# Kernel tuning notes

Measured on AMD Instinct MI355X. Metric: run time of the kernel, lower is better.

The kernel has to match this reference:

```python
import jax, jax.numpy as jnp
import numpy as np

BS, EMB, RES = 256, 768, 14
N_MASKS, HID, OUT, N_PROJ = 16, 4096, 256, 4
BN_EPS = 1e-5


def setup_inputs() -> dict:
    key = jax.random.key(0)
    ks = jax.random.split(key, 8)
    x = jax.random.normal(ks[0], (BS, EMB, RES, RES), jnp.float32)
    # binary ROI masks over the 14x14 = 196 patch grid
    masks = (jax.random.uniform(ks[1], (BS, N_MASKS, RES * RES)) < 0.3).astype(jnp.float32)
    projection_idx = jax.random.randint(ks[2], (N_MASKS,), 0, N_PROJ, jnp.int32)
    mask_ids = jax.random.randint(ks[3], (BS, N_MASKS), 0, 100, jnp.int32)
    # stacked params for the N_PROJ MLP projectors
    W1 = jax.random.normal(ks[4], (N_PROJ, EMB, HID), jnp.float32) * 0.02
    b1 = jnp.zeros((N_PROJ, HID), jnp.float32)
    gamma = jnp.ones((N_PROJ, HID), jnp.float32)
    beta = jnp.zeros((N_PROJ, HID), jnp.float32)
    W2 = jax.random.normal(ks[5], (N_PROJ, HID, OUT), jnp.float32) * 0.02
    b2 = jnp.zeros((N_PROJ, OUT), jnp.float32)
    return {"x": x, "masks": masks, "projection_idx": projection_idx,
            "mask_ids": mask_ids, "W1": W1, "b1": b1, "gamma": gamma,
            "beta": beta, "W2": W2, "b2": b2}


def reference(x, masks, projection_idx, mask_ids, W1, b1, gamma, beta, W2, b2):
    bs, emb, hx, hy = x.shape
    # [bs, emb, hx, hy] -> [bs, hw, emb]
    emb_local = jnp.transpose(x, (0, 2, 3, 1)).reshape(bs, hx * hy, emb)
    # mask-normalized pooling:  pooled[b,n,:] = mean of embeddings inside mask n
    area = masks.sum(axis=-1, keepdims=True)
    smpl = masks / jnp.maximum(area, 1.0)
    pooled = smpl @ emb_local                       # [bs, n_masks, emb]
    # dense dispatch: run EVERY projector over all pooled tokens (as original)
    h = jnp.einsum('bne,peh->pbnh', pooled, W1) + b1[:, None, None, :]
    # BatchNorm1d in training mode over flattened (bs*n_masks) batch, per projector
    mu = h.mean(axis=(1, 2), keepdims=True)
    var = jnp.mean(jnp.square(h - mu), axis=(1, 2), keepdims=True)  # biased var
    h = (h - mu) * jax.lax.rsqrt(var + BN_EPS) * gamma[:, None, None, :] + beta[:, None, None, :]
    h = jax.nn.relu(h)
    o = jnp.einsum('pbnh,pho->pbno', h, W2) + b2[:, None, None, :]   # [P, bs, n, out]
    # keep only projector projection_idx[n] for mask-slot n (disjoint selection)
    n_proj = W1.shape[0]
    sel = (projection_idx[None, :] == jnp.arange(n_proj)[:, None]).astype(o.dtype)  # [P, n]
    xs = (o * sel[:, None, :, None]).sum(axis=0)     # [bs, n_masks, out]
    return (xs, mask_ids)
```

## Files before the change

### kernel.cpp

```cpp
#include <hip/hip_runtime.h>
#include <hip/hip_bf16.h>

#define BS 256
#define EMB 768
#define HW 196
#define NMASK 16
#define HID 4096
#define OUT 256
#define NPROJ 4
#define MROWS 4096

typedef __attribute__((ext_vector_type(8))) short bf16x8;
typedef __attribute__((ext_vector_type(4))) float f32x4;
typedef __attribute__((ext_vector_type(8))) unsigned short u16x8;

__device__ inline float bf2f(unsigned short u) {
    unsigned int x = ((unsigned int)u) << 16;
    return __builtin_bit_cast(float, x);
}
__device__ inline short f2bfs(float f) {
    return __builtin_bit_cast(short, __float2bfloat16(f));
}

#define GL16(gptr, lptr)                                                     \
    __builtin_amdgcn_global_load_lds(                                        \
        (const __attribute__((address_space(1))) void*)(gptr),               \
        (__attribute__((address_space(3))) void*)(lptr), 16, 0, 0)

__global__ __launch_bounds__(256) void pool_mfma(
    const float* __restrict__ x, const float* __restrict__ masks,
    __hip_bfloat16* __restrict__ pooledG)
{
    __shared__ __align__(16) short afr[7 * 64 * 8];
    __shared__ float inv[NMASK];
    const int ec = blockIdx.x, b = blockIdx.y, tid = threadIdx.x;
    const float* mb = masks + (size_t)b * NMASK * HW;

    for (int s = tid; s < 7 * 64; s += 256) {
        int m = s & 15, kb = ((s >> 4) & 3) * 8 + (s >> 6) * 32;
        short v[8];
        #pragma unroll
        for (int j = 0; j < 8; ++j) {
            int kk = kb + j;
            v[j] = (kk < HW) ? f2bfs(mb[m * HW + kk]) : (short)0;
        }
        #pragma unroll
        for (int j = 0; j < 8; ++j) afr[s * 8 + j] = v[j];
    }
    if (tid >= 192) {
        int l = tid - 192, m = l >> 2, q = l & 3;
        float a = 0.f;
        for (int hw = q; hw < HW; hw += 4) a += mb[m * HW + hw];
        a += __shfl_xor(a, 1);
        a += __shfl_xor(a, 2);
        if (q == 0) inv[m] = 1.0f / fmaxf(a, 1.0f);
    }
    __syncthreads();

    const int lane = tid & 63, w = tid >> 6;
    const int lc = lane & 15, l4 = lane >> 4;
    const int ebase = ec * 192 + w * 48;
    const bf16x8* afv = (const bf16x8*)afr;
    f32x4 acc[3] = {};

    const float* xb0 = x + ((size_t)b * EMB + ebase + lc) * HW;

    for (int kc = 0; kc < 6; ++kc) {
        bf16x8 af = afv[kc * 64 + lane];
        float4 u[3][2];
        #pragma unroll
        for (int t = 0; t < 3; ++t) {
            const float* xr = xb0 + (size_t)(t * 16) * HW + kc * 32 + l4 * 8;
            u[t][0] = *(const float4*)(xr);
            u[t][1] = *(const float4*)(xr + 4);
        }
        #pragma unroll
        for (int t = 0; t < 3; ++t) {
            bf16x8 bf;
            bf[0] = f2bfs(u[t][0].x); bf[1] = f2bfs(u[t][0].y);
            bf[2] = f2bfs(u[t][0].z); bf[3] = f2bfs(u[t][0].w);
            bf[4] = f2bfs(u[t][1].x); bf[5] = f2bfs(u[t][1].y);
            bf[6] = f2bfs(u[t][1].z); bf[7] = f2bfs(u[t][1].w);
            acc[t] = __builtin_amdgcn_mfma_f32_16x16x32_bf16(af, bf, acc[t], 0, 0, 0);
        }
    }
    {
        bf16x8 af = afv[6 * 64 + lane];
        #pragma unroll
        for (int t = 0; t < 3; ++t) {
            bf16x8 bf = {};
            if (l4 == 0) {
                float4 u0 = *(const float4*)(xb0 + (size_t)(t * 16) * HW + 192);
                bf[0] = f2bfs(u0.x); bf[1] = f2bfs(u0.y);
                bf[2] = f2bfs(u0.z); bf[3] = f2bfs(u0.w);
            }
            acc[t] = __builtin_amdgcn_mfma_f32_16x16x32_bf16(af, bf, acc[t], 0, 0, 0);
        }
    }

    #pragma unroll
    for (int t = 0; t < 3; ++t) {
        int e = ebase + t * 16 + lc;
        #pragma unroll
        for (int j = 0; j < 4; ++j) {
            int m = l4 * 4 + j;
            pooledG[((size_t)m * 256 + b) * EMB + e] =
                __float2bfloat16(acc[t][j] * inv[m]);
        }
    }
}

__global__ __launch_bounds__(256) void transpose_cvt(
    const float* __restrict__ src, __hip_bfloat16* __restrict__ dst, int R, int C)
{
    __shared__ float tile[64][65];
    const float* s = src + (size_t)blockIdx.z * R * C;
    __hip_bfloat16* d = dst + (size_t)blockIdx.z * R * C;
    const int c0 = blockIdx.x * 64, r0 = blockIdx.y * 64, tid = threadIdx.x;
    for (int i = tid; i < 4096; i += 256) {
        int r = i >> 6, c = i & 63;
        tile[r][c] = s[(size_t)(r0 + r) * C + c0 + c];
    }
    __syncthreads();
    for (int i = tid; i < 4096; i += 256) {
        int c = i >> 6, r = i & 63;
        d[(size_t)(c0 + c) * R + r0 + r] = __float2bfloat16(tile[r][c]);
    }
}

__global__ __launch_bounds__(256) void transpose_pg(
    const __hip_bfloat16* __restrict__ src, __hip_bfloat16* __restrict__ dst)
{
    __shared__ __hip_bfloat16 tile[64][65];
    const int c0 = blockIdx.x * 64, r0 = blockIdx.y * 64, tid = threadIdx.x;
    for (int i = tid; i < 4096; i += 256) {
        int r = i >> 6, c = i & 63;
        tile[r][c] = src[(size_t)(r0 + r) * EMB + c0 + c];
    }
    __syncthreads();
    for (int i = tid; i < 4096; i += 256) {
        int c = i >> 6, r = i & 63;
        dst[(size_t)(c0 + c) * MROWS + r0 + r] = tile[r][c];
    }
}

__global__ __launch_bounds__(256) void meanpool(
    const __hip_bfloat16* __restrict__ PT, float* __restrict__ mp)
{
    const int e = blockIdx.x, tid = threadIdx.x;
    const u16x8* p = (const u16x8*)(PT + (size_t)e * MROWS);
    u16x8 v1 = p[tid], v2 = p[tid + 256];
    float s = 0.f;
    #pragma unroll
    for (int j = 0; j < 8; ++j) s += bf2f((unsigned short)v1[j]) + bf2f((unsigned short)v2[j]);
    #pragma unroll
    for (int o = 1; o < 64; o <<= 1) s += __shfl_xor(s, o);
    __shared__ float wsum[4];
    if ((tid & 63) == 0) wsum[tid >> 6] = s;
    __syncthreads();
    if (tid == 0) mp[e] = (wsum[0] + wsum[1] + wsum[2] + wsum[3]) * (1.0f / 4096.0f);
}

__global__ __launch_bounds__(256) void cgemm(
    const __hip_bfloat16* __restrict__ PT, float* __restrict__ Cf)
{
    __shared__ __align__(16) __hip_bfloat16 As[128 * 32];
    __shared__ __align__(16) __hip_bfloat16 Bs[128 * 32];
    const int tid = threadIdx.x, lane = tid & 63, wid = tid >> 6;
    const int n0 = blockIdx.x * 128, m0 = blockIdx.y * 128, kbase = blockIdx.z * 512;
    const int wr = wid >> 1, wc = wid & 1;
    const int l4 = lane >> 4, lc = lane & 15;

    f32x4 acc[4][4] = {};
    for (int k0 = kbase; k0 < kbase + 512; k0 += 32) {
        __syncthreads();
        #pragma unroll
        for (int r = 0; r < 2; ++r) {
            int t = r * 256 + tid;
            int row = t >> 2, ko = (t & 3) * 8;
            GL16(PT + (size_t)(m0 + row) * MROWS + k0 + ko, &As[(r * 256 + wid * 64) * 8]);
        }
        #pragma unroll
        for (int r = 0; r < 2; ++r) {
            int t = r * 256 + tid;
            int row = t >> 2, ko = (t & 3) * 8;
            GL16(PT + (size_t)(n0 + row) * MROWS + k0 + ko, &Bs[(r * 256 + wid * 64) * 8]);
        }
        __syncthreads();
        const bf16x8* Av = (const bf16x8*)As;
        const bf16x8* Bv = (const bf16x8*)Bs;
        bf16x8 a[4], b[4];
        #pragma unroll
        for (int m = 0; m < 4; ++m) a[m] = Av[(wr * 64 + m * 16 + lc) * 4 + l4];
        #pragma unroll
        for (int n = 0; n < 4; ++n) b[n] = Bv[(wc * 64 + n * 16 + lc) * 4 + l4];
        #pragma unroll
        for (int m = 0; m < 4; ++m)
            #pragma unroll
            for (int n = 0; n < 4; ++n)
                acc[m][n] = __builtin_amdgcn_mfma_f32_16x16x32_bf16(a[m], b[n], acc[m][n], 0, 0, 0);
    }
    #pragma unroll
    for (int m = 0; m < 4; ++m)
        #pragma unroll
        for (int n = 0; n < 4; ++n)
            #pragma unroll
            for (int j = 0; j < 4; ++j) {
                int row = m0 + wr * 64 + m * 16 + l4 * 4 + j;
                int col = n0 + wc * 64 + n * 16 + lc;
                atomicAdd(&Cf[(size_t)row * EMB + col], acc[m][n][j]);
            }
}

__global__ __launch_bounds__(256) void cvt_c(
    const float* __restrict__ Cf, __hip_bfloat16* __restrict__ Cbf)
{
    int i = (blockIdx.x * 256 + threadIdx.x) * 4;
    float4 v = *(const float4*)(Cf + i);
    const float s = 1.0f / 4096.0f;
    Cbf[i + 0] = __float2bfloat16(v.x * s);
    Cbf[i + 1] = __float2bfloat16(v.y * s);
    Cbf[i + 2] = __float2bfloat16(v.z * s);
    Cbf[i + 3] = __float2bfloat16(v.w * s);
}

__global__ __launch_bounds__(256) void ugemm(
    const __hip_bfloat16* __restrict__ W1T, const __hip_bfloat16* __restrict__ Cbf,
    const float* __restrict__ mp,
    float* __restrict__ Eh2, float* __restrict__ Mu)
{
    __shared__ __align__(16) __hip_bfloat16 As[128 * 32];
    __shared__ __align__(16) __hip_bfloat16 Bs[128 * 32];
    const int tid = threadIdx.x, lane = tid & 63, wid = tid >> 6;
    const int n0 = blockIdx.x * 128, m0 = blockIdx.y * 128, p = blockIdx.z;
    const __hip_bfloat16* Ap = W1T + (size_t)p * HID * EMB;
    const int wr = wid >> 1, wc = wid & 1;
    const int l4 = lane >> 4, lc = lane & 15;

    f32x4 acc[4][4] = {};
    for (int k0 = 0; k0 < EMB; k0 += 32) {
        __syncthreads();
        #pragma unroll
        for (int r = 0; r < 2; ++r) {
            int t = r * 256 + tid;
            int row = t >> 2, ko = (t & 3) * 8;
            GL16(Ap + (size_t)(m0 + row) * EMB + k0 + ko, &As[(r * 256 + wid * 64) * 8]);
        }
        #pragma unroll
        for (int r = 0; r < 2; ++r) {
            int t = r * 256 + tid;
            int row = t >> 2, ko = (t & 3) * 8;
            GL16(Cbf + (size_t)(n0 + row) * EMB + k0 + ko, &Bs[(r * 256 + wid * 64) * 8]);
        }
        __syncthreads();
        const bf16x8* Av = (const bf16x8*)As;
        const bf16x8* Bv = (const bf16x8*)Bs;
        bf16x8 a[4], b[4];
        #pragma unroll
        for (int m = 0; m < 4; ++m) a[m] = Av[(wr * 64 + m * 16 + lc) * 4 + l4];
        #pragma unroll
        for (int n = 0; n < 4; ++n) b[n] = Bv[(wc * 64 + n * 16 + lc) * 4 + l4];
        #pragma unroll
        for (int m = 0; m < 4; ++m)
            #pragma unroll
            for (int n = 0; n < 4; ++n)
                acc[m][n] = __builtin_amdgcn_mfma_f32_16x16x32_bf16(a[m], b[n], acc[m][n], 0, 0, 0);
    }

    float mpv[4];
    #pragma unroll
    for (int n = 0; n < 4; ++n) mpv[n] = mp[n0 + wc * 64 + n * 16 + lc];
    #pragma unroll
    for (int m = 0; m < 4; ++m) {
        #pragma unroll
        for (int j = 0; j < 4; ++j) {
            int row = m0 + wr * 64 + m * 16 + l4 * 4 + j;
            const __hip_bfloat16* wrow = Ap + (size_t)row * EMB;
            float e2 = 0.f, mu = 0.f;
            #pragma unroll
            for (int n = 0; n < 4; ++n) {
                int col = n0 + wc * 64 + n * 16 + lc;
                float wv = bf2f(__builtin_bit_cast(unsigned short, wrow[col]));
                e2 += acc[m][n][j] * wv;
                mu += mpv[n] * wv;
            }
            e2 += __shfl_xor(e2, 1); e2 += __shfl_xor(e2, 2);
            e2 += __shfl_xor(e2, 4); e2 += __shfl_xor(e2, 8);
            mu += __shfl_xor(mu, 1); mu += __shfl_xor(mu, 2);
            mu += __shfl_xor(mu, 4); mu += __shfl_xor(mu, 8);
            if (lc == 0) {
                atomicAdd(&Eh2[p * HID + row], e2);
                atomicAdd(&Mu [p * HID + row], mu);
            }
        }
    }
}

__global__ __launch_bounds__(256) void finalize(
    const float* __restrict__ Eh2, const float* __restrict__ Mu,
    const float* __restrict__ gamma, const float* __restrict__ beta,
    float* __restrict__ sbuf, float* __restrict__ tbuf)
{
    int i = blockIdx.x * 256 + threadIdx.x;
    float mu  = Mu[i];
    float var = Eh2[i] - mu * mu;
    float is  = rsqrtf(fmaxf(var, 0.0f) + 1e-5f);
    float sc  = gamma[i] * is;
    sbuf[i] = sc;
    tbuf[i] = beta[i] - mu * sc;
}

__global__ __launch_bounds__(256) void gemm1_sel(
    const __hip_bfloat16* __restrict__ A, const __hip_bfloat16* __restrict__ W1T,
    const int* __restrict__ proj,
    const float* __restrict__ sbuf, const float* __restrict__ tbuf,
    __hip_bfloat16* __restrict__ hrelu)
{
    __shared__ __align__(16) __hip_bfloat16 As[128 * 32];
    __shared__ __align__(16) __hip_bfloat16 Bs[128 * 32];
    const int tid = threadIdx.x, lane = tid & 63, wid = tid >> 6;
    const int n0 = blockIdx.x * 128, m0 = blockIdx.y * 128;
    const int p = proj[blockIdx.y >> 1];
    const __hip_bfloat16* Bp = W1T + (size_t)p * HID * EMB;
    const int wr = wid >> 1, wc = wid & 1;
    const int l4 = lane >> 4, lc = lane & 15;

    f32x4 acc[4][4] = {};
    for (int k0 = 0; k0 < EMB; k0 += 32) {
        __syncthreads();
        #pragma unroll
        for (int r = 0; r < 2; ++r) {
            int t = r * 256 + tid;
            int row = t >> 2, ko = (t & 3) * 8;
            GL16(A + (size_t)(m0 + row) * EMB + k0 + ko, &As[(r * 256 + wid * 64) * 8]);
        }
        #pragma unroll
        for (int r = 0; r < 2; ++r) {
            int t = r * 256 + tid;
            int row = t >> 2, ko = (t & 3) * 8;
            GL16(Bp + (size_t)(n0 + row) * EMB + k0 + ko, &Bs[(r * 256 + wid * 64) * 8]);
        }
        __syncthreads();
        const bf16x8* Av = (const bf16x8*)As;
        const bf16x8* Bv = (const bf16x8*)Bs;
        bf16x8 a[4], b[4];
        #pragma unroll
        for (int m = 0; m < 4; ++m) a[m] = Av[(wr * 64 + m * 16 + lc) * 4 + l4];
        #pragma unroll
        for (int n = 0; n < 4; ++n) b[n] = Bv[(wc * 64 + n * 16 + lc) * 4 + l4];
        #pragma unroll
        for (int m = 0; m < 4; ++m)
            #pragma unroll
            for (int n = 0; n < 4; ++n)
                acc[m][n] = __builtin_amdgcn_mfma_f32_16x16x32_bf16(a[m], b[n], acc[m][n], 0, 0, 0);
    }

    #pragma unroll
    for (int n = 0; n < 4; ++n) {
        int col = n0 + wc * 64 + n * 16 + lc;
        float s = sbuf[p * HID + col];
        float t = tbuf[p * HID + col];
        #pragma unroll
        for (int m = 0; m < 4; ++m)
            #pragma unroll
            for (int j = 0; j < 4; ++j) {
                int row = m0 + wr * 64 + m * 16 + l4 * 4 + j;
                float v = fmaxf(acc[m][n][j] * s + t, 0.0f);
                hrelu[(size_t)row * HID + col] = __float2bfloat16(v);
            }
    }
}

__global__ __launch_bounds__(256) void gemm2(
    const __hip_bfloat16* __restrict__ Hn, const __hip_bfloat16* __restrict__ W2T,
    const int* __restrict__ proj, const float* __restrict__ b2,
    float* __restrict__ out)
{
    __shared__ __align__(16) __hip_bfloat16 As[64 * 32];
    __shared__ __align__(16) __hip_bfloat16 Bs[64 * 32];
    const int tid = threadIdx.x, lane = tid & 63, wid = tid >> 6;
    const int nmask = blockIdx.x;
    const int bc    = blockIdx.y;
    const int ct    = blockIdx.z >> 2, kz = blockIdx.z & 3;
    const int p = proj[nmask];
    const __hip_bfloat16* Ap = Hn + (size_t)(nmask * 256 + bc * 64) * HID;
    const __hip_bfloat16* Bp = W2T + ((size_t)p * OUT + ct * 64) * HID;
    const int wr = wid >> 1, wc = wid & 1;
    const int l4 = lane >> 4, lc = lane & 15;

    f32x4 acc[2][2] = {};
    for (int k0 = kz * 1024; k0 < kz * 1024 + 1024; k0 += 32) {
        __syncthreads();
        {
            int row = tid >> 2, ko = (tid & 3) * 8;
            GL16(Ap + (size_t)row * HID + k0 + ko, &As[(wid * 64) * 8]);
            GL16(Bp + (size_t)row * HID + k0 + ko, &Bs[(wid * 64) * 8]);
        }
        __syncthreads();
        const bf16x8* Av = (const bf16x8*)As;
        const bf16x8* Bv = (const bf16x8*)Bs;
        bf16x8 a[2], b[2];
        a[0] = Av[(wr * 32 +      lc) * 4 + l4];
        a[1] = Av[(wr * 32 + 16 + lc) * 4 + l4];
        b[0] = Bv[(wc * 32 +      lc) * 4 + l4];
        b[1] = Bv[(wc * 32 + 16 + lc) * 4 + l4];
        #pragma unroll
        for (int m = 0; m < 2; ++m)
            #pragma unroll
            for (int n = 0; n < 2; ++n)
                acc[m][n] = __builtin_amdgcn_mfma_f32_16x16x32_bf16(a[m], b[n], acc[m][n], 0, 0, 0);
    }

    #pragma unroll
    for (int m = 0; m < 2; ++m)
        #pragma unroll
        for (int n = 0; n < 2; ++n)
            #pragma unroll
            for (int j = 0; j < 4; ++j) {
                int bb = bc * 64 + wr * 32 + m * 16 + l4 * 4 + j;
                int oc = ct * 64 + wc * 32 + n * 16 + lc;
                float v = acc[m][n][j] + (kz == 0 ? b2[p * OUT + oc] : 0.0f);
                atomicAdd(&out[((size_t)bb * NMASK + nmask) * OUT + oc], v);
            }
}

__global__ __launch_bounds__(256) void tail_ids(const int* __restrict__ mids,
                                                float* __restrict__ out)
{
    int i = blockIdx.x * 256 + threadIdx.x;
    out[(size_t)MROWS * OUT + i] = (float)mids[i];
}

extern "C" void kernel_launch(void* const* d_in, const int* in_sizes, int n_in,
                              void* d_out, int out_size, void* d_ws, size_t ws_size,
                              hipStream_t stream)
{
    const float* x     = (const float*)d_in[0];
    const float* masks = (const float*)d_in[1];
    const int*   proj  = (const int*)d_in[2];
    const int*   mids  = (const int*)d_in[3];
    const float* W1    = (const float*)d_in[4];
    const float* gamma = (const float*)d_in[6];
    const float* beta  = (const float*)d_in[7];
    const float* W2    = (const float*)d_in[8];
    const float* b2    = (const float*)d_in[9];
    float* out = (float*)d_out;

    char* ws = (char*)d_ws;
    __hip_bfloat16* pooledG = (__hip_bfloat16*)(ws);
    __hip_bfloat16* W1T     = (__hip_bfloat16*)(ws + 6291456);
    __hip_bfloat16* W2T     = (__hip_bfloat16*)(ws + 31457280);
    float*          mp      = (float*)(ws + 39845888);
    float*          Eh2     = (float*)(ws + 39848960);
    float*          Mu      = (float*)(ws + 39914496);
    float*          sbuf    = (float*)(ws + 39980032);
    float*          tbuf    = (float*)(ws + 40045568);
    char* R = ws + 40111104;
    __hip_bfloat16* pooledT = (__hip_bfloat16*)(R);
    float*          Cf      = (float*)(R + 6291456);
    __hip_bfloat16* Cbf     = (__hip_bfloat16*)(R + 8650752);
    __hip_bfloat16* hrelu   = (__hip_bfloat16*)(R);

    hipMemsetAsync(Eh2, 0, 2 * NPROJ * HID * sizeof(float), stream);
    hipMemsetAsync(Cf, 0, EMB * EMB * sizeof(float), stream);
    hipMemsetAsync(out, 0, (size_t)MROWS * OUT * sizeof(float), stream);

    pool_mfma<<<dim3(4, BS), 256, 0, stream>>>(x, masks, pooledG);
    transpose_cvt<<<dim3(HID / 64, EMB / 64, NPROJ), 256, 0, stream>>>(W1, W1T, EMB, HID);
    transpose_cvt<<<dim3(OUT / 64, HID / 64, NPROJ), 256, 0, stream>>>(W2, W2T, HID, OUT);
    transpose_pg<<<dim3(EMB / 64, MROWS / 64), 256, 0, stream>>>(pooledG, pooledT);
    meanpool<<<EMB, 256, 0, stream>>>(pooledT, mp);
    cgemm<<<dim3(6, 6, 8), 256, 0, stream>>>(pooledT, Cf);
    cvt_c<<<(EMB * EMB) / 1024, 256, 0, stream>>>(Cf, Cbf);
    ugemm<<<dim3(6, 32, 4), 256, 0, stream>>>(W1T, Cbf, mp, Eh2, Mu);
    finalize<<<(NPROJ * HID) / 256, 256, 0, stream>>>(Eh2, Mu, gamma, beta, sbuf, tbuf);
    gemm1_sel<<<dim3(HID / 128, MROWS / 128), 256, 0, stream>>>(pooledG, W1T, proj, sbuf, tbuf, hrelu);
    gemm2<<<dim3(NMASK, BS / 64, 16), 256, 0, stream>>>(hrelu, W2T, proj, b2, out);
    tail_ids<<<(BS * NMASK) / 256, 256, 0, stream>>>(mids, out);
}
```

Baseline: 232.7 us.

## Replace atomic split-K accumulation with partial buffers and separate reductions

The split-K outputs of cgemm, ugemm and gemm2 now go with plain stores into per-slice partial buffers instead of global atomicAdds. The partials are summed in cvt_c, finalize and a new reduce_out kernel, which also adds the bias and writes the mask ids. This removes three memsets and the atomic contention. In exchange it adds extra workspace and roughly doubles global traffic for the partial buffers (about 19 MB for C and 16 MB for the output).

Result: faster. 211.6 us (-9.1%).

```diff
diff --git a/kernel.cpp b/kernel.cpp
--- a/kernel.cpp
+++ b/kernel.cpp
@@ -162,12 +162,13 @@
 }
 
 __global__ __launch_bounds__(256) void cgemm(
-    const __hip_bfloat16* __restrict__ PT, float* __restrict__ Cf)
+    const __hip_bfloat16* __restrict__ PT, float* __restrict__ Cpart)
 {
     __shared__ __align__(16) __hip_bfloat16 As[128 * 32];
     __shared__ __align__(16) __hip_bfloat16 Bs[128 * 32];
     const int tid = threadIdx.x, lane = tid & 63, wid = tid >> 6;
     const int n0 = blockIdx.x * 128, m0 = blockIdx.y * 128, kbase = blockIdx.z * 512;
+    float* Cp = Cpart + (size_t)blockIdx.z * EMB * EMB;
     const int wr = wid >> 1, wc = wid & 1;
     const int l4 = lane >> 4, lc = lane & 15;
 
@@ -208,26 +209,31 @@
             for (int j = 0; j < 4; ++j) {
                 int row = m0 + wr * 64 + m * 16 + l4 * 4 + j;
                 int col = n0 + wc * 64 + n * 16 + lc;
-                atomicAdd(&Cf[(size_t)row * EMB + col], acc[m][n][j]);
+                Cp[(size_t)row * EMB + col] = acc[m][n][j];
             }
 }
 
 __global__ __launch_bounds__(256) void cvt_c(
-    const float* __restrict__ Cf, __hip_bfloat16* __restrict__ Cbf)
+    const float* __restrict__ Cpart, __hip_bfloat16* __restrict__ Cbf)
 {
     int i = (blockIdx.x * 256 + threadIdx.x) * 4;
-    float4 v = *(const float4*)(Cf + i);
+    float sx = 0.f, sy = 0.f, sz = 0.f, sw = 0.f;
+    #pragma unroll
+    for (int kz = 0; kz < 8; ++kz) {
+        float4 v = *(const float4*)(Cpart + (size_t)kz * EMB * EMB + i);
+        sx += v.x; sy += v.y; sz += v.z; sw += v.w;
+    }
     const float s = 1.0f / 4096.0f;
-    Cbf[i + 0] = __float2bfloat16(v.x * s);
-    Cbf[i + 1] = __float2bfloat16(v.y * s);
-    Cbf[i + 2] = __float2bfloat16(v.z * s);
-    Cbf[i + 3] = __float2bfloat16(v.w * s);
+    Cbf[i + 0] = __float2bfloat16(sx * s);
+    Cbf[i + 1] = __float2bfloat16(sy * s);
+    Cbf[i + 2] = __float2bfloat16(sz * s);
+    Cbf[i + 3] = __float2bfloat16(sw * s);
 }
 
 __global__ __launch_bounds__(256) void ugemm(
     const __hip_bfloat16* __restrict__ W1T, const __hip_bfloat16* __restrict__ Cbf,
     const float* __restrict__ mp,
-    float* __restrict__ Eh2, float* __restrict__ Mu)
+    float* __restrict__ Eh2p, float* __restrict__ Mup)
 {
     __shared__ __align__(16) __hip_bfloat16 As[128 * 32];
     __shared__ __align__(16) __hip_bfloat16 Bs[128 * 32];
@@ -289,21 +295,27 @@
             mu += __shfl_xor(mu, 1); mu += __shfl_xor(mu, 2);
             mu += __shfl_xor(mu, 4); mu += __shfl_xor(mu, 8);
             if (lc == 0) {
-                atomicAdd(&Eh2[p * HID + row], e2);
-                atomicAdd(&Mu [p * HID + row], mu);
+                size_t idx = (((size_t)blockIdx.x * 2 + wc) * NPROJ + p) * HID + row;
+                Eh2p[idx] = e2;
+                Mup [idx] = mu;
             }
         }
     }
 }
 
 __global__ __launch_bounds__(256) void finalize(
-    const float* __restrict__ Eh2, const float* __restrict__ Mu,
+    const float* __restrict__ Eh2p, const float* __restrict__ Mup,
     const float* __restrict__ gamma, const float* __restrict__ beta,
     float* __restrict__ sbuf, float* __restrict__ tbuf)
 {
     int i = blockIdx.x * 256 + threadIdx.x;
-    float mu  = Mu[i];
-    float var = Eh2[i] - mu * mu;
+    float e2 = 0.f, mu = 0.f;
+    #pragma unroll
+    for (int bx = 0; bx < 12; ++bx) {
+        e2 += Eh2p[bx * (NPROJ * HID) + i];
+        mu += Mup [bx * (NPROJ * HID) + i];
+    }
+    float var = e2 - mu * mu;
     float is  = rsqrtf(fmaxf(var, 0.0f) + 1e-5f);
     float sc  = gamma[i] * is;
     sbuf[i] = sc;
@@ -373,8 +385,7 @@
 
 __global__ __launch_bounds__(256) void gemm2(
     const __hip_bfloat16* __restrict__ Hn, const __hip_bfloat16* __restrict__ W2T,
-    const int* __restrict__ proj, const float* __restrict__ b2,
-    float* __restrict__ out)
+    const int* __restrict__ proj, float* __restrict__ Opart)
 {
     __shared__ __align__(16) __hip_bfloat16 As[64 * 32];
     __shared__ __align__(16) __hip_bfloat16 Bs[64 * 32];
@@ -385,6 +396,7 @@
     const int p = proj[nmask];
     const __hip_bfloat16* Ap = Hn + (size_t)(nmask * 256 + bc * 64) * HID;
     const __hip_bfloat16* Bp = W2T + ((size_t)p * OUT + ct * 64) * HID;
+    float* Op = Opart + (size_t)kz * MROWS * OUT;
     const int wr = wid >> 1, wc = wid & 1;
     const int l4 = lane >> 4, lc = lane & 15;
 
@@ -419,16 +431,32 @@
             for (int j = 0; j < 4; ++j) {
                 int bb = bc * 64 + wr * 32 + m * 16 + l4 * 4 + j;
                 int oc = ct * 64 + wc * 32 + n * 16 + lc;
-                float v = acc[m][n][j] + (kz == 0 ? b2[p * OUT + oc] : 0.0f);
-                atomicAdd(&out[((size_t)bb * NMASK + nmask) * OUT + oc], v);
+                Op[((size_t)bb * NMASK + nmask) * OUT + oc] = acc[m][n][j];
             }
 }
 
-__global__ __launch_bounds__(256) void tail_ids(const int* __restrict__ mids,
-                                                float* __restrict__ out)
-{
-    int i = blockIdx.x * 256 + threadIdx.x;
-    out[(size_t)MROWS * OUT + i] = (float)mids[i];
+__global__ __launch_bounds__(256) void reduce_out(
+    const float* __restrict__ Opart, const float* __restrict__ b2,
+    const int* __restrict__ proj, const int* __restrict__ mids,
+    float* __restrict__ out)
+{
+    int i = (blockIdx.x * 256 + threadIdx.x) * 4;
+    float sx = 0.f, sy = 0.f, sz = 0.f, sw = 0.f;
+    #pragma unroll
+    for (int kz = 0; kz < 4; ++kz) {
+        float4 v = *(const float4*)(Opart + (size_t)kz * MROWS * OUT + i);
+        sx += v.x; sy += v.y; sz += v.z; sw += v.w;
+    }
+    int nm = (i >> 8) & 15;
+    int p  = proj[nm];
+    float4 bv = *(const float4*)(b2 + p * OUT + (i & 255));
+    float4 r;
+    r.x = sx + bv.x; r.y = sy + bv.y; r.z = sz + bv.z; r.w = sw + bv.w;
+    *(float4*)(out + i) = r;
+    if (blockIdx.x < 16) {
+        int t = blockIdx.x * 256 + threadIdx.x;
+        out[(size_t)MROWS * OUT + t] = (float)mids[t];
+    }
 }
 
 extern "C" void kernel_launch(void* const* d_in, const int* in_sizes, int n_in,
@@ -451,30 +479,27 @@
     __hip_bfloat16* W1T     = (__hip_bfloat16*)(ws + 6291456);
     __hip_bfloat16* W2T     = (__hip_bfloat16*)(ws + 31457280);
     float*          mp      = (float*)(ws + 39845888);
-    float*          Eh2     = (float*)(ws + 39848960);
-    float*          Mu      = (float*)(ws + 39914496);
-    float*          sbuf    = (float*)(ws + 39980032);
-    float*          tbuf    = (float*)(ws + 40045568);
-    char* R = ws + 40111104;
+    float*          Eh2p    = (float*)(ws + 39848960);
+    float*          Mup     = (float*)(ws + 40635392);
+    float*          sbuf    = (float*)(ws + 41421824);
+    float*          tbuf    = (float*)(ws + 41487360);
+    char* R = ws + 41552896;
     __hip_bfloat16* pooledT = (__hip_bfloat16*)(R);
-    float*          Cf      = (float*)(R + 6291456);
-    __hip_bfloat16* Cbf     = (__hip_bfloat16*)(R + 8650752);
+    float*          Cpart   = (float*)(R + 6291456);
+    __hip_bfloat16* Cbf     = (__hip_bfloat16*)(R + 25165824);
     __hip_bfloat16* hrelu   = (__hip_bfloat16*)(R);
-
-    hipMemsetAsync(Eh2, 0, 2 * NPROJ * HID * sizeof(float), stream);
-    hipMemsetAsync(Cf, 0, EMB * EMB * sizeof(float), stream);
-    hipMemsetAsync(out, 0, (size_t)MROWS * OUT * sizeof(float), stream);
+    float*          Opart   = (float*)(R + 33554432);
 
     pool_mfma<<<dim3(4, BS), 256, 0, stream>>>(x, masks, pooledG);
     transpose_cvt<<<dim3(HID / 64, EMB / 64, NPROJ), 256, 0, stream>>>(W1, W1T, EMB, HID);
     transpose_cvt<<<dim3(OUT / 64, HID / 64, NPROJ), 256, 0, stream>>>(W2, W2T, HID, OUT);
     transpose_pg<<<dim3(EMB / 64, MROWS / 64), 256, 0, stream>>>(pooledG, pooledT);
     meanpool<<<EMB, 256, 0, stream>>>(pooledT, mp);
-    cgemm<<<dim3(6, 6, 8), 256, 0, stream>>>(pooledT, Cf);
-    cvt_c<<<(EMB * EMB) / 1024, 256, 0, stream>>>(Cf, Cbf);
-    ugemm<<<dim3(6, 32, 4), 256, 0, stream>>>(W1T, Cbf, mp, Eh2, Mu);
-    finalize<<<(NPROJ * HID) / 256, 256, 0, stream>>>(Eh2, Mu, gamma, beta, sbuf, tbuf);
+    cgemm<<<dim3(6, 6, 8), 256, 0, stream>>>(pooledT, Cpart);
+    cvt_c<<<(EMB * EMB) / 1024, 256, 0, stream>>>(Cpart, Cbf);
+    ugemm<<<dim3(6, 32, 4), 256, 0, stream>>>(W1T, Cbf, mp, Eh2p, Mup);
+    finalize<<<(NPROJ * HID) / 256, 256, 0, stream>>>(Eh2p, Mup, gamma, beta, sbuf, tbuf);
     gemm1_sel<<<dim3(HID / 128, MROWS / 128), 256, 0, stream>>>(pooledG, W1T, proj, sbuf, tbuf, hrelu);
-    gemm2<<<dim3(NMASK, BS / 64, 16), 256, 0, stream>>>(hrelu, W2T, proj, b2, out);
-    tail_ids<<<(BS * NMASK) / 256, 256, 0, stream>>>(mids, out);
-}
+    gemm2<<<dim3(NMASK, BS / 64, 16), 256, 0, stream>>>(hrelu, W2T, proj, Opart);
+    reduce_out<<<(MROWS * OUT) / 1024, 256, 0, stream>>>(Opart, b2, proj, mids, out);
+}
```
